# Kernel optimization log

Hardware: AMD Instinct MI355X
Metric: run time of the kernel (lower is better)

Reference implementation:

```python
import jax, jax.numpy as jnp
import numpy as np

N_NODES = 50000
N_EDGES_UND = 400000
N_GRAPHS = 128
LATENT = 64
OUT_DIM = 64
NODE_F = 64
EDGE_F = 32
MAX_LV = 3


def setup_inputs() -> dict:
    key = jax.random.key(0)
    ks = jax.random.split(key, 12)
    rng = np.random.default_rng(0)
    # Build consistent directed edge list: each undirected pair (u,v) yields
    # directed edges e (u->v) and e+E_und (v->u); rev maps each to its twin.
    u = rng.integers(0, N_NODES, size=N_EDGES_UND)
    v = rng.integers(0, N_NODES, size=N_EDGES_UND)
    src = jnp.asarray(np.concatenate([u, v]), dtype=jnp.int32)
    dst = jnp.asarray(np.concatenate([v, u]), dtype=jnp.int32)
    e = np.arange(N_EDGES_UND)
    rev = jnp.asarray(np.concatenate([e + N_EDGES_UND, e]), dtype=jnp.int32)
    graph_ids = jnp.sort(jax.random.randint(ks[0], (N_NODES,), 0, N_GRAPHS)).astype(jnp.int32)
    s = 0.05
    return {
        'node_feat': jax.random.normal(ks[1], (N_NODES, NODE_F), jnp.float32),
        'edge_feat': jax.random.normal(ks[2], (2 * N_EDGES_UND, EDGE_F), jnp.float32),
        'src': src, 'dst': dst, 'rev': rev,
        'graph_ids': graph_ids, 'n_graphs': N_GRAPHS,
        'Wn': jax.random.normal(ks[3], (NODE_F, LATENT), jnp.float32) * s,
        'bn': jnp.zeros((LATENT,), jnp.float32),
        'We': jax.random.normal(ks[4], (EDGE_F, LATENT), jnp.float32) * s,
        'be': jnp.zeros((LATENT,), jnp.float32),
        'Wc': jax.random.normal(ks[5], (LATENT, LATENT), jnp.float32) * s,
        'bc': jnp.zeros((LATENT,), jnp.float32),
        'Wo': jax.random.normal(ks[6], (LATENT, OUT_DIM), jnp.float32) * s,
        'bo': jnp.zeros((OUT_DIM,), jnp.float32),
    }


def reference(node_feat, edge_feat, src, dst, rev, graph_ids, n_graphs,
              Wn, bn, We, be, Wc, bc, Wo, bo):
    n_nodes = node_feat.shape[0]
    # w_n2l / w_e2l
    input_node_linear = node_feat @ Wn + bn                  # [N, D]
    input_edge_linear = edge_feat @ We + be                  # [E, D]
    # n2e spmm: each directed edge gathers its source node's row
    input_message = input_edge_linear + input_node_linear[src]  # [E, D]
    cur = jax.nn.relu(input_message)
    # loopy BP: e2e spmm = (sum of messages into src node) - reverse-edge message
    for _ in range(MAX_LV):
        node_agg = jax.ops.segment_sum(cur, dst, num_segments=n_nodes)  # [N, D]
        e2epool = node_agg[src] - cur[rev]                              # [E, D]
        cur = jax.nn.relu(e2epool @ Wc + bc + input_message)
    # e2n spmm: sum incoming edge messages per node
    e2npool = jax.ops.segment_sum(cur, dst, num_segments=n_nodes)       # [N, D]
    hidden_msg = jax.nn.relu(e2npool)
    reluact = jax.nn.relu(hidden_msg @ Wo + bo)                         # [N, out]
    # subg spmm: sum node outputs per graph
    y = jax.ops.segment_sum(reluact, graph_ids, num_segments=n_graphs)  # [G, out]
    return jax.nn.relu(y)
```

## Files before the change

### kernel.cpp

```cpp
#include <hip/hip_runtime.h>


#define NN 50000
#define NE 800000
#define NG 128
#define D 64
#define LDE 36
#define LDW 66
#define LDO 72

typedef unsigned short u16;
typedef unsigned int u32;
typedef __bf16 bf16x8 __attribute__((ext_vector_type(8)));
typedef float f32x4 __attribute__((ext_vector_type(4)));

__device__ __forceinline__ float b2f(u16 u){ u32 x=((u32)u)<<16; float f; __builtin_memcpy(&f,&x,4); return f; }
__device__ __forceinline__ u16 f2b(float f){ u32 x; __builtin_memcpy(&x,&f,4); x += 0x7fffu + ((x>>16)&1u); return (u16)(x>>16); }
__device__ __forceinline__ u32 pack2(float a, float b){ return (u32)f2b(a) | ((u32)f2b(b)<<16); }
__device__ __forceinline__ void unpack8(uint4 v, float* o){
  o[0]=b2f((u16)(v.x&0xffffu)); o[1]=b2f((u16)(v.x>>16));
  o[2]=b2f((u16)(v.y&0xffffu)); o[3]=b2f((u16)(v.y>>16));
  o[4]=b2f((u16)(v.z&0xffffu)); o[5]=b2f((u16)(v.z>>16));
  o[6]=b2f((u16)(v.w&0xffffu)); o[7]=b2f((u16)(v.w>>16));
}

__global__ __launch_bounds__(256) void k_prep(const float* __restrict__ Wc, const float* __restrict__ We,
                                              u16* __restrict__ wcB, u16* __restrict__ weB){
  int i = blockIdx.x*256 + threadIdx.x;
  if (i < 4096){
    int nt = i>>10, r = i&1023;
    int h = r>>9, r2 = r&511;
    int j = r2>>3, kk = r2&7;
    int row = nt*16 + (j&15);
    int k = h*32 + (j>>4)*8 + kk;
    wcB[i] = f2b(Wc[k*D + row]);
  }
  int t = i - 4096;
  if (t >= 0 && t < 2048){
    int nt = t>>9, r = t&511;
    int j = r>>3, kk = r&7;
    int row = nt*16 + (j&15);
    int k = (j>>4)*8 + kk;
    weB[t] = f2b(We[k*D + row]);
  }
}

template<int ZERO>
__global__ __launch_bounds__(256) void k_cvt(const float* __restrict__ srcv, u16* __restrict__ dstb,
                                             float* __restrict__ zbuf){
  size_t i = (size_t)(blockIdx.x*256 + threadIdx.x)*4;
  float4 v = *(const float4*)(srcv + i);
  *(uint2*)(dstb + i) = make_uint2(pack2(v.x,v.y), pack2(v.z,v.w));
  if (ZERO) *(float4*)(zbuf + i) = make_float4(0.f,0.f,0.f,0.f);
}

__global__ __launch_bounds__(256) void k_inl(const float* __restrict__ nf, const float* __restrict__ Wn,
                                             const float* __restrict__ bn, u16* __restrict__ inlb){
  __shared__ float w[D*D];
  for (int i=threadIdx.x;i<D*D;i+=256) w[i]=Wn[i];
  __syncthreads();
  const int d = threadIdx.x&63;
  const int n = blockIdx.x*4 + (threadIdx.x>>6);
  if (n>=NN) return;
  float v = bn[d];
  const float* row = nf + (size_t)n*D;
  #pragma unroll 8
  for (int k=0;k<D;k++) v += row[k]*w[k*D+d];
  inlb[(size_t)n*D+d] = f2b(v);
}

__global__ __launch_bounds__(256) void k_im(const float* __restrict__ ef, const u16* __restrict__ weB,
                                            const float* __restrict__ be, const u16* __restrict__ inlb,
                                            const int* __restrict__ src, const int* __restrict__ perm,
                                            u16* __restrict__ imP){
  __shared__ __align__(16) u16 efs[64*LDE];
  __shared__ float os[64*68];
  const int t = threadIdx.x;
  const int ebase = blockIdx.x*64;
  {
    int e=t>>2, k0=(t&3)*8;
    const float* p = ef + (size_t)(ebase+e)*32 + k0;
    float4 v0=*(const float4*)p, v1=*(const float4*)(p+4);
    uint4 pk = make_uint4(pack2(v0.x,v0.y),pack2(v0.z,v0.w),pack2(v1.x,v1.y),pack2(v1.z,v1.w));
    *(uint4*)&efs[e*LDE + k0] = pk;
  }
  {
    int w=t>>6, lane=t&63, q=lane>>4, mr=lane&15;
    int rowb=w*16;
    bf16x8 A = *(const bf16x8*)&efs[(rowb+mr)*LDE + q*8];
    #pragma unroll
    for (int nt=0;nt<4;nt++){
      bf16x8 B = *(const bf16x8*)(weB + nt*512 + lane*8);
      f32x4 acc = {0.f,0.f,0.f,0.f};
      acc = __builtin_amdgcn_mfma_f32_16x16x32_bf16(A,B,acc,0,0,0);
      #pragma unroll
      for (int r=0;r<4;r++) os[(rowb+q*4+r)*68 + nt*16+mr] = acc[r];
    }
  }
  {
    int e=t>>2, d0=(t&3)*16;
    const size_t eg = (size_t)(ebase+e);
    const int s = src[eg], ps = perm[eg];
    const u16* ip = inlb + (size_t)s*D + d0;
    uint4 iv0 = *(const uint4*)ip, iv1 = *(const uint4*)(ip+8);
    float il[16]; unpack8(iv0,il); unpack8(iv1,il+8);
    float x[16];
    #pragma unroll
    for (int j=0;j<16;j++) x[j] = os[e*68 + d0 + j] + be[d0+j] + il[j];
    uint4 p0 = make_uint4(pack2(x[0],x[1]),pack2(x[2],x[3]),pack2(x[4],x[5]),pack2(x[6],x[7]));
    uint4 p1 = make_uint4(pack2(x[8],x[9]),pack2(x[10],x[11]),pack2(x[12],x[13]),pack2(x[14],x[15]));
    u16* op = imP + (size_t)ps*D + d0;
    *(uint4*)op = p0; *(uint4*)(op+8) = p1;
  }
}

template<int MODE>
__global__ __launch_bounds__(256) void k_iter(const u16* __restrict__ imP, const u16* __restrict__ revIn,
      const u16* __restrict__ naWb, const u16* __restrict__ wcB, const float* __restrict__ bc,
      const int* __restrict__ srcP, const int* __restrict__ prevP, const int* __restrict__ nodeP,
      u16* __restrict__ revOut, float* __restrict__ naW_out){
  __shared__ __align__(16) u16 xs[64*LDW];
  __shared__ __align__(16) u16 os[64*LDO];
  __shared__ int nid[64];
  const int t = threadIdx.x;
  const int lane = t&63, w = t>>6;
  const size_t sbase = (size_t)blockIdx.x*64;
  if (lane < 16) nid[w*16 + lane] = nodeP[sbase + w*16 + lane];
  {
    const int e = t>>2, d0 = (t&3)*16;
    const size_t slot = sbase + e;
    const u16* ip = imP + slot*D + d0;
    uint4 r0 = *(const uint4*)ip, r1 = *(const uint4*)(ip+8);
    float x[16]; unpack8(r0,x); unpack8(r1,x+8);
    if (MODE == 1){
      const int sp = srcP[slot];
      const u16* cp = revIn + slot*D + d0;
      uint4 c0=*(const uint4*)cp, c1=*(const uint4*)(cp+8);
      const u16* np_ = naWb + (size_t)sp*D + d0;
      uint4 n0=*(const uint4*)np_, n1=*(const uint4*)(np_+8);
      float cv[16], nv[16];
      unpack8(c0,cv); unpack8(c1,cv+8);
      unpack8(n0,nv); unpack8(n1,nv+8);
      #pragma unroll
      for (int j=0;j<16;j++) x[j] += nv[j] - cv[j] + bc[d0+j];
    }
    #pragma unroll
    for (int j=0;j<16;j++) x[j] = x[j]>0.f ? x[j] : 0.f;
    uint4 p0 = make_uint4(pack2(x[0],x[1]),pack2(x[2],x[3]),pack2(x[4],x[5]),pack2(x[6],x[7]));
    uint4 p1 = make_uint4(pack2(x[8],x[9]),pack2(x[10],x[11]),pack2(x[12],x[13]),pack2(x[14],x[15]));
    u16* qd = &xs[e*LDW + d0];
    *(uint4*)qd = p0; *(uint4*)(qd+8) = p1;
  }
  {
    const int q = lane>>4, mr = lane&15;
    const int rowb = w*16;
    bf16x8 A0 = *(const bf16x8*)&xs[(rowb+mr)*LDW + q*8];
    bf16x8 A1 = *(const bf16x8*)&xs[(rowb+mr)*LDW + 32 + q*8];
    #pragma unroll
    for (int nt=0;nt<4;nt++){
      bf16x8 B0 = *(const bf16x8*)(wcB + nt*1024 + lane*8);
      bf16x8 B1 = *(const bf16x8*)(wcB + nt*1024 + 512 + lane*8);
      f32x4 acc = {0.f,0.f,0.f,0.f};
      acc = __builtin_amdgcn_mfma_f32_16x16x32_bf16(A0,B0,acc,0,0,0);
      acc = __builtin_amdgcn_mfma_f32_16x16x32_bf16(A1,B1,acc,0,0,0);
      #pragma unroll
      for (int r=0;r<4;r++) os[(rowb+q*4+r)*LDO + nt*16 + mr] = f2b(acc[r]);
    }
    const int lr = lane>>2, cc = lane&3;
    const int tgt = prevP[sbase + rowb + lr];
    u16* gp = revOut + (size_t)tgt*D + cc*16;
    *(uint4*)gp     = *(const uint4*)&os[(rowb+lr)*LDO + cc*16];
    *(uint4*)(gp+8) = *(const uint4*)&os[(rowb+lr)*LDO + cc*16 + 8];
    float acc = 0.f;
    int curn = nid[rowb];
    #pragma unroll 4
    for (int i=0;i<16;++i){
      int n = nid[rowb+i];
      if (n != curn){
        atomicAdd(&naW_out[(size_t)curn*D + lane], acc);
        curn = n; acc = 0.f;
      }
      acc += b2f(os[(rowb+i)*LDO + lane]);
    }
    atomicAdd(&naW_out[(size_t)curn*D + lane], acc);
  }
}

__global__ __launch_bounds__(256) void k_last(const u16* __restrict__ imP, const u16* __restrict__ revIn,
      const u16* __restrict__ naWb, const float* __restrict__ bc,
      const int* __restrict__ srcP, const int* __restrict__ nodeP,
      float* __restrict__ e2n){
  __shared__ __align__(16) u16 xs[64*LDW];
  __shared__ int nid[64];
  const int t = threadIdx.x;
  const int lane = t&63, w = t>>6;
  const size_t sbase = (size_t)blockIdx.x*64;
  if (lane < 16) nid[w*16+lane] = nodeP[sbase + w*16 + lane];
  {
    const int e = t>>2, d0 = (t&3)*16;
    const size_t slot = sbase + e;
    const u16* ip = imP + slot*D + d0;
    uint4 r0 = *(const uint4*)ip, r1 = *(const uint4*)(ip+8);
    float x[16]; unpack8(r0,x); unpack8(r1,x+8);
    const int sp = srcP[slot];
    const u16* cp = revIn + slot*D + d0;
    uint4 c0 = *(const uint4*)cp, c1 = *(const uint4*)(cp+8);
    const u16* np_ = naWb + (size_t)sp*D + d0;
    uint4 n0 = *(const uint4*)np_, n1 = *(const uint4*)(np_+8);
    float cv[16], nv[16];
    unpack8(c0,cv); unpack8(c1,cv+8);
    unpack8(n0,nv); unpack8(n1,nv+8);
    #pragma unroll
    for (int j=0;j<16;j++){ x[j] += nv[j] - cv[j] + bc[d0+j]; x[j] = x[j]>0.f ? x[j] : 0.f; }
    uint4 p0 = make_uint4(pack2(x[0],x[1]),pack2(x[2],x[3]),pack2(x[4],x[5]),pack2(x[6],x[7]));
    uint4 p1 = make_uint4(pack2(x[8],x[9]),pack2(x[10],x[11]),pack2(x[12],x[13]),pack2(x[14],x[15]));
    u16* qd = &xs[e*LDW + d0];
    *(uint4*)qd = p0; *(uint4*)(qd+8) = p1;
  }
  {
    float acc = 0.f;
    int curn = nid[w*16];
    #pragma unroll 4
    for (int i=0;i<16;++i){
      int n = nid[w*16+i];
      if (n != curn){
        atomicAdd(&e2n[(size_t)curn*D + lane], acc);
        curn = n; acc = 0.f;
      }
      acc += b2f(xs[(w*16+i)*LDW + lane]);
    }
    atomicAdd(&e2n[(size_t)curn*D + lane], acc);
  }
}

__global__ void k_hist(const int* __restrict__ dst, int* __restrict__ cnt){
  int e = blockIdx.x*256 + threadIdx.x;
  atomicAdd(&cnt[dst[e]], 1);
}
__global__ __launch_bounds__(1024) void k_scan1(const int* __restrict__ cnt, int* __restrict__ outv,
                                                int* __restrict__ bsums, int n){
  __shared__ int sh[1024];
  int i = blockIdx.x*1024 + threadIdx.x;
  int v = (i<n)? cnt[i] : 0;
  sh[threadIdx.x]=v;
  __syncthreads();
  for (int off=1; off<1024; off<<=1){
    int tv = (threadIdx.x>=(unsigned)off)? sh[threadIdx.x-off] : 0;
    __syncthreads();
    sh[threadIdx.x] += tv;
    __syncthreads();
  }
  if (i<n) outv[i] = sh[threadIdx.x] - v;
  if (threadIdx.x==1023) bsums[blockIdx.x] = sh[1023];
}
__global__ __launch_bounds__(1024) void k_scan3(int* __restrict__ off, int* __restrict__ cur,
                                                const int* __restrict__ bsums, int n){
  __shared__ int spref;
  if (threadIdx.x < 64){
    int v = ((int)threadIdx.x < (int)blockIdx.x) ? bsums[threadIdx.x] : 0;
    #pragma unroll
    for (int o=1;o<64;o<<=1) v += __shfl_xor(v, o, 64);
    if (threadIdx.x==0) spref = v;
  }
  __syncthreads();
  int i = blockIdx.x*1024 + threadIdx.x;
  if (i<n){ int v = off[i] + spref; off[i]=v; cur[i]=v; }
}
__global__ void k_fill(const int* __restrict__ dst, const int* __restrict__ src,
                       int* __restrict__ cur, int* __restrict__ perm,
                       int* __restrict__ srcP, int* __restrict__ nodeP){
  int e = blockIdx.x*256 + threadIdx.x;
  int d = dst[e];
  int pos = atomicAdd(&cur[d], 1);
  perm[e] = pos;
  srcP[pos] = src[e];
  nodeP[pos] = d;
}
__global__ void k_prev(const int* __restrict__ rev, const int* __restrict__ perm, int* __restrict__ prevP){
  int e = blockIdx.x*256 + threadIdx.x;
  prevP[perm[e]] = perm[rev[e]];
}

__global__ __launch_bounds__(256) void k_final(const float* __restrict__ e2n, const float* __restrict__ Wo,
                                               const float* __restrict__ bo, const int* __restrict__ gid,
                                               float* __restrict__ yacc){
  __shared__ float w[D*D];
  for (int i=threadIdx.x;i<D*D;i+=256) w[i]=Wo[i];
  __syncthreads();
  const int d = threadIdx.x&63, sub = threadIdx.x>>6;
  const int n0 = blockIdx.x*32 + sub*8;
  const float bod = bo[d];
  float acc=0.f; int curg=-1;
  for (int i=0;i<8;i++){
    int n=n0+i;
    if (n>=NN) break;
    int g = gid[n];
    if (g!=curg){ if (curg>=0) atomicAdd(&yacc[curg*D+d], acc); curg=g; acc=0.f; }
    float v=bod;
    const float* er = e2n + (size_t)n*D;
    #pragma unroll 8
    for (int k=0;k<D;k++){ float h=er[k]; h = h>0.f?h:0.f; v += h*w[k*D+d]; }
    acc += (v>0.f ? v : 0.f);
  }
  if (curg>=0) atomicAdd(&yacc[curg*D+d], acc);
}
__global__ void k_out(const float* __restrict__ yacc, float* __restrict__ outp){
  int i = blockIdx.x*256 + threadIdx.x;
  if (i<NG*D){ float v=yacc[i]; outp[i]= v>0.f?v:0.f; }
}

static constexpr size_t SZ_E   = (size_t)NE*D*2;
static constexpr size_t SZ_NF4 = (size_t)NN*D*4;
static constexpr size_t SZ_NB  = (size_t)NN*D*2;
static constexpr size_t OFF_IMP  = 0;
static constexpr size_t OFF_RVA  = SZ_E;
static constexpr size_t OFF_RVB  = 2*SZ_E;
static constexpr size_t OFF_CCUR = 3*SZ_E;
static constexpr size_t OFF_NA0  = OFF_CCUR + 200064;
static constexpr size_t OFF_NA1  = OFF_NA0 + SZ_NF4;
static constexpr size_t OFF_E2N  = OFF_NA1 + SZ_NF4;
static constexpr size_t OFF_YACC = OFF_E2N + SZ_NF4;
static constexpr size_t ZERO_SZ  = 200064 + 3*SZ_NF4 + (size_t)NG*D*4;
static constexpr size_t OFF_NAB  = OFF_YACC + (size_t)NG*D*4;
static constexpr size_t OFF_INL  = OFF_NAB + SZ_NB;
static constexpr size_t OFF_COFF = OFF_INL + SZ_NB;
static constexpr size_t OFF_PERM = OFF_COFF + 200064;
static constexpr size_t OFF_SRCP = OFF_PERM + (size_t)NE*4;
static constexpr size_t OFF_PRVP = OFF_SRCP + (size_t)NE*4;
static constexpr size_t OFF_NODP = OFF_PRVP + (size_t)NE*4;
static constexpr size_t OFF_BS   = OFF_NODP + (size_t)NE*4;
static constexpr size_t OFF_WCT  = OFF_BS + 256;
static constexpr size_t OFF_WET  = OFF_WCT + 8192;

extern "C" void kernel_launch(void* const* d_in, const int* in_sizes, int n_in,
                              void* d_out, int out_size, void* d_ws, size_t ws_size,
                              hipStream_t stream) {
  const float* node_feat = (const float*)d_in[0];
  const float* edge_feat = (const float*)d_in[1];
  const int*   src       = (const int*)d_in[2];
  const int*   dst       = (const int*)d_in[3];
  const int*   rev       = (const int*)d_in[4];
  const int*   gid       = (const int*)d_in[5];
  const float* Wn = (const float*)d_in[7];
  const float* bn = (const float*)d_in[8];
  const float* We = (const float*)d_in[9];
  const float* be = (const float*)d_in[10];
  const float* Wc = (const float*)d_in[11];
  const float* bc = (const float*)d_in[12];
  const float* Wo = (const float*)d_in[13];
  const float* bo = (const float*)d_in[14];

  char* ws = (char*)d_ws;
  u16*   imP     = (u16*)(ws + OFF_IMP);
  u16*   revA    = (u16*)(ws + OFF_RVA);
  u16*   revB    = (u16*)(ws + OFF_RVB);
  float* naW0    = (float*)(ws + OFF_NA0);
  float* naW1    = (float*)(ws + OFF_NA1);
  float* e2n     = (float*)(ws + OFF_E2N);
  float* yacc    = (float*)(ws + OFF_YACC);
  u16*   naWb    = (u16*)(ws + OFF_NAB);
  u16*   inlb    = (u16*)(ws + OFF_INL);
  int*   csr_off = (int*)(ws + OFF_COFF);
  int*   csr_cur = (int*)(ws + OFF_CCUR);
  int*   perm    = (int*)(ws + OFF_PERM);
  int*   srcP    = (int*)(ws + OFF_SRCP);
  int*   prevP   = (int*)(ws + OFF_PRVP);
  int*   nodeP   = (int*)(ws + OFF_NODP);
  int*   bsums   = (int*)(ws + OFF_BS);
  u16*   wcB     = (u16*)(ws + OFF_WCT);
  u16*   weB     = (u16*)(ws + OFF_WET);

  hipMemsetAsync(ws + OFF_CCUR, 0, ZERO_SZ, stream);

  k_hist <<<NE/256, 256, 0, stream>>>(dst, csr_cur);
  k_scan1<<<49, 1024, 0, stream>>>(csr_cur, csr_off, bsums, NN);
  k_scan3<<<49, 1024, 0, stream>>>(csr_off, csr_cur, bsums, NN);
  k_fill <<<NE/256, 256, 0, stream>>>(dst, src, csr_cur, perm, srcP, nodeP);
  k_prev <<<NE/256, 256, 0, stream>>>(rev, perm, prevP);

  k_prep<<<24, 256, 0, stream>>>(Wc, We, wcB, weB);
  k_inl <<<NN/4, 256, 0, stream>>>(node_feat, Wn, bn, inlb);
  k_im  <<<NE/64, 256, 0, stream>>>(edge_feat, weB, be, inlb, src, perm, imP);

  k_iter<0><<<NE/64, 256, 0, stream>>>(imP, revA, naWb, wcB, bc, srcP, prevP, nodeP, revA, naW0);
  k_cvt<0><<<3125, 256, 0, stream>>>(naW0, naWb, (float*)nullptr);
  k_iter<1><<<NE/64, 256, 0, stream>>>(imP, revA, naWb, wcB, bc, srcP, prevP, nodeP, revB, naW1);
  k_cvt<1><<<3125, 256, 0, stream>>>(naW1, naWb, naW0);
  k_iter<1><<<NE/64, 256, 0, stream>>>(imP, revB, naWb, wcB, bc, srcP, prevP, nodeP, revA, naW0);
  k_cvt<0><<<3125, 256, 0, stream>>>(naW0, naWb, (float*)nullptr);
  k_last<<<NE/64, 256, 0, stream>>>(imP, revA, naWb, bc, srcP, nodeP, e2n);

  k_final<<<(NN+31)/32, 256, 0, stream>>>(e2n, Wo, bo, gid, yacc);
  k_out<<<(NG*D)/256, 256, 0, stream>>>(yacc, (float*)d_out);
}
```

Baseline: 674.4 us.

## Replace atomic scatter aggregation with CSR pull-gather and pair-interleaved in-place edge updates

New measurement: 712.3 us. +5.6%, slower.

```diff
diff --git a/kernel.cpp b/kernel.cpp
--- a/kernel.cpp
+++ b/kernel.cpp
@@ -3,6 +3,7 @@
 
 #define NN 50000
 #define NE 800000
+#define NEU 400000
 #define NG 128
 #define D 64
 #define LDE 36
@@ -43,15 +44,6 @@
     int k = (j>>4)*8 + kk;
     weB[t] = f2b(We[k*D + row]);
   }
-}
-
-template<int ZERO>
-__global__ __launch_bounds__(256) void k_cvt(const float* __restrict__ srcv, u16* __restrict__ dstb,
-                                             float* __restrict__ zbuf){
-  size_t i = (size_t)(blockIdx.x*256 + threadIdx.x)*4;
-  float4 v = *(const float4*)(srcv + i);
-  *(uint2*)(dstb + i) = make_uint2(pack2(v.x,v.y), pack2(v.z,v.w));
-  if (ZERO) *(float4*)(zbuf + i) = make_float4(0.f,0.f,0.f,0.f);
 }
 
 __global__ __launch_bounds__(256) void k_inl(const float* __restrict__ nf, const float* __restrict__ Wn,
@@ -69,24 +61,24 @@
   inlb[(size_t)n*D+d] = f2b(v);
 }
 
-__global__ __launch_bounds__(256) void k_im(const float* __restrict__ ef, const u16* __restrict__ weB,
-                                            const float* __restrict__ be, const u16* __restrict__ inlb,
-                                            const int* __restrict__ src, const int* __restrict__ perm,
-                                            u16* __restrict__ imP){
+__global__ __launch_bounds__(256) void k_imf(const float* __restrict__ ef, const u16* __restrict__ weB,
+        const float* __restrict__ be, const u16* __restrict__ inlb, const int* __restrict__ src,
+        const u16* __restrict__ wcB, u16* __restrict__ imP, u16* __restrict__ yv){
   __shared__ __align__(16) u16 efs[64*LDE];
-  __shared__ float os[64*68];
+  __shared__ float osf[64*68];
+  __shared__ __align__(16) u16 xs[64*LDW];
+  __shared__ __align__(16) u16 osb[64*LDO];
   const int t = threadIdx.x;
+  const int lane = t&63, w = t>>6;
   const int ebase = blockIdx.x*64;
   {
     int e=t>>2, k0=(t&3)*8;
     const float* p = ef + (size_t)(ebase+e)*32 + k0;
     float4 v0=*(const float4*)p, v1=*(const float4*)(p+4);
-    uint4 pk = make_uint4(pack2(v0.x,v0.y),pack2(v0.z,v0.w),pack2(v1.x,v1.y),pack2(v1.z,v1.w));
-    *(uint4*)&efs[e*LDE + k0] = pk;
-  }
-  {
-    int w=t>>6, lane=t&63, q=lane>>4, mr=lane&15;
-    int rowb=w*16;
+    *(uint4*)&efs[e*LDE+k0] = make_uint4(pack2(v0.x,v0.y),pack2(v0.z,v0.w),pack2(v1.x,v1.y),pack2(v1.z,v1.w));
+  }
+  {
+    int q=lane>>4, mr=lane&15, rowb=w*16;
     bf16x8 A = *(const bf16x8*)&efs[(rowb+mr)*LDE + q*8];
     #pragma unroll
     for (int nt=0;nt<4;nt++){
@@ -94,61 +86,80 @@
       f32x4 acc = {0.f,0.f,0.f,0.f};
       acc = __builtin_amdgcn_mfma_f32_16x16x32_bf16(A,B,acc,0,0,0);
       #pragma unroll
-      for (int r=0;r<4;r++) os[(rowb+q*4+r)*68 + nt*16+mr] = acc[r];
+      for (int r=0;r<4;r++) osf[(rowb+q*4+r)*68 + nt*16+mr] = acc[r];
     }
   }
   {
     int e=t>>2, d0=(t&3)*16;
     const size_t eg = (size_t)(ebase+e);
-    const int s = src[eg], ps = perm[eg];
+    const int s = src[eg];
     const u16* ip = inlb + (size_t)s*D + d0;
     uint4 iv0 = *(const uint4*)ip, iv1 = *(const uint4*)(ip+8);
     float il[16]; unpack8(iv0,il); unpack8(iv1,il+8);
     float x[16];
     #pragma unroll
-    for (int j=0;j<16;j++) x[j] = os[e*68 + d0 + j] + be[d0+j] + il[j];
+    for (int j=0;j<16;j++) x[j] = osf[e*68 + d0 + j] + be[d0+j] + il[j];
     uint4 p0 = make_uint4(pack2(x[0],x[1]),pack2(x[2],x[3]),pack2(x[4],x[5]),pack2(x[6],x[7]));
     uint4 p1 = make_uint4(pack2(x[8],x[9]),pack2(x[10],x[11]),pack2(x[12],x[13]),pack2(x[14],x[15]));
-    u16* op = imP + (size_t)ps*D + d0;
+    u16* op = imP + eg*D + d0;
     *(uint4*)op = p0; *(uint4*)(op+8) = p1;
-  }
-}
-
-template<int MODE>
-__global__ __launch_bounds__(256) void k_iter(const u16* __restrict__ imP, const u16* __restrict__ revIn,
+    #pragma unroll
+    for (int j=0;j<16;j++) x[j] = x[j]>0.f ? x[j] : 0.f;
+    uint4 q0 = make_uint4(pack2(x[0],x[1]),pack2(x[2],x[3]),pack2(x[4],x[5]),pack2(x[6],x[7]));
+    uint4 q1 = make_uint4(pack2(x[8],x[9]),pack2(x[10],x[11]),pack2(x[12],x[13]),pack2(x[14],x[15]));
+    u16* qd = &xs[e*LDW + d0];
+    *(uint4*)qd = q0; *(uint4*)(qd+8) = q1;
+  }
+  {
+    const int q=lane>>4, mr=lane&15, rowb=w*16;
+    bf16x8 A0 = *(const bf16x8*)&xs[(rowb+mr)*LDW + q*8];
+    bf16x8 A1 = *(const bf16x8*)&xs[(rowb+mr)*LDW + 32 + q*8];
+    #pragma unroll
+    for (int nt=0;nt<4;nt++){
+      bf16x8 B0 = *(const bf16x8*)(wcB + nt*1024 + lane*8);
+      bf16x8 B1 = *(const bf16x8*)(wcB + nt*1024 + 512 + lane*8);
+      f32x4 acc = {0.f,0.f,0.f,0.f};
+      acc = __builtin_amdgcn_mfma_f32_16x16x32_bf16(A0,B0,acc,0,0,0);
+      acc = __builtin_amdgcn_mfma_f32_16x16x32_bf16(A1,B1,acc,0,0,0);
+      #pragma unroll
+      for (int r=0;r<4;r++) osb[(rowb+q*4+r)*LDO + nt*16 + mr] = f2b(acc[r]);
+    }
+    const int lr = lane>>2, cc = lane&3;
+    u16* gp = yv + (size_t)(ebase+rowb+lr)*D + cc*16;
+    *(uint4*)gp     = *(const uint4*)&osb[(rowb+lr)*LDO + cc*16];
+    *(uint4*)(gp+8) = *(const uint4*)&osb[(rowb+lr)*LDO + cc*16 + 8];
+  }
+}
+
+__global__ __launch_bounds__(256) void k_iter_pi(const u16* __restrict__ imP, u16* __restrict__ yv,
       const u16* __restrict__ naWb, const u16* __restrict__ wcB, const float* __restrict__ bc,
-      const int* __restrict__ srcP, const int* __restrict__ prevP, const int* __restrict__ nodeP,
-      u16* __restrict__ revOut, float* __restrict__ naW_out){
+      const int* __restrict__ src){
   __shared__ __align__(16) u16 xs[64*LDW];
   __shared__ __align__(16) u16 os[64*LDO];
-  __shared__ int nid[64];
   const int t = threadIdx.x;
   const int lane = t&63, w = t>>6;
-  const size_t sbase = (size_t)blockIdx.x*64;
-  if (lane < 16) nid[w*16 + lane] = nodeP[sbase + w*16 + lane];
-  {
-    const int e = t>>2, d0 = (t&3)*16;
-    const size_t slot = sbase + e;
-    const u16* ip = imP + slot*D + d0;
-    uint4 r0 = *(const uint4*)ip, r1 = *(const uint4*)(ip+8);
-    float x[16]; unpack8(r0,x); unpack8(r1,x+8);
-    if (MODE == 1){
-      const int sp = srcP[slot];
-      const u16* cp = revIn + slot*D + d0;
-      uint4 c0=*(const uint4*)cp, c1=*(const uint4*)(cp+8);
-      const u16* np_ = naWb + (size_t)sp*D + d0;
-      uint4 n0=*(const uint4*)np_, n1=*(const uint4*)(np_+8);
-      float cv[16], nv[16];
-      unpack8(c0,cv); unpack8(c1,cv+8);
-      unpack8(n0,nv); unpack8(n1,nv+8);
-      #pragma unroll
-      for (int j=0;j<16;j++) x[j] += nv[j] - cv[j] + bc[d0+j];
-    }
-    #pragma unroll
-    for (int j=0;j<16;j++) x[j] = x[j]>0.f ? x[j] : 0.f;
+  const int pbase = blockIdx.x*32 + w*8;
+  {
+    const int rr = lane>>2, d0 = (lane&3)*16;
+    const int pr = pbase + (rr&7);
+    const int e   = (rr<8)? pr : NEU+pr;
+    const int etw = (rr<8)? NEU+pr : pr;
+    const int sp = src[e];
+    const u16* ip = imP + (size_t)e*D + d0;
+    uint4 r0=*(const uint4*)ip, r1=*(const uint4*)(ip+8);
+    const u16* cp = yv + (size_t)etw*D + d0;
+    uint4 c0=*(const uint4*)cp, c1=*(const uint4*)(cp+8);
+    const u16* np_ = naWb + (size_t)sp*D + d0;
+    uint4 n0=*(const uint4*)np_, n1=*(const uint4*)(np_+8);
+    float x[16], cv[16], nv[16];
+    unpack8(r0,x); unpack8(r1,x+8);
+    unpack8(c0,cv); unpack8(c1,cv+8);
+    unpack8(n0,nv); unpack8(n1,nv+8);
+    #pragma unroll
+    for (int j=0;j<16;j++){ x[j] += nv[j] - cv[j] + bc[d0+j]; x[j] = x[j]>0.f ? x[j] : 0.f; }
     uint4 p0 = make_uint4(pack2(x[0],x[1]),pack2(x[2],x[3]),pack2(x[4],x[5]),pack2(x[6],x[7]));
     uint4 p1 = make_uint4(pack2(x[8],x[9]),pack2(x[10],x[11]),pack2(x[12],x[13]),pack2(x[14],x[15]));
-    u16* qd = &xs[e*LDW + d0];
+    u16* qd = &xs[(w*16+rr)*LDW + d0];
     *(uint4*)qd = p0; *(uint4*)(qd+8) = p1;
   }
   {
@@ -167,70 +178,70 @@
       for (int r=0;r<4;r++) os[(rowb+q*4+r)*LDO + nt*16 + mr] = f2b(acc[r]);
     }
     const int lr = lane>>2, cc = lane&3;
-    const int tgt = prevP[sbase + rowb + lr];
-    u16* gp = revOut + (size_t)tgt*D + cc*16;
+    const int pr2 = pbase + (lr&7);
+    const int e2 = (lr<8)? pr2 : NEU+pr2;
+    u16* gp = yv + (size_t)e2*D + cc*16;
     *(uint4*)gp     = *(const uint4*)&os[(rowb+lr)*LDO + cc*16];
     *(uint4*)(gp+8) = *(const uint4*)&os[(rowb+lr)*LDO + cc*16 + 8];
-    float acc = 0.f;
-    int curn = nid[rowb];
-    #pragma unroll 4
-    for (int i=0;i<16;++i){
-      int n = nid[rowb+i];
-      if (n != curn){
-        atomicAdd(&naW_out[(size_t)curn*D + lane], acc);
-        curn = n; acc = 0.f;
-      }
-      acc += b2f(os[(rowb+i)*LDO + lane]);
-    }
-    atomicAdd(&naW_out[(size_t)curn*D + lane], acc);
-  }
-}
-
-__global__ __launch_bounds__(256) void k_last(const u16* __restrict__ imP, const u16* __restrict__ revIn,
-      const u16* __restrict__ naWb, const float* __restrict__ bc,
-      const int* __restrict__ srcP, const int* __restrict__ nodeP,
-      float* __restrict__ e2n){
-  __shared__ __align__(16) u16 xs[64*LDW];
-  __shared__ int nid[64];
+  }
+}
+
+__global__ __launch_bounds__(256) void k_last_pi(const u16* __restrict__ imP, u16* __restrict__ yv,
+      const u16* __restrict__ naWb, const float* __restrict__ bc, const int* __restrict__ src){
   const int t = threadIdx.x;
   const int lane = t&63, w = t>>6;
-  const size_t sbase = (size_t)blockIdx.x*64;
-  if (lane < 16) nid[w*16+lane] = nodeP[sbase + w*16 + lane];
-  {
-    const int e = t>>2, d0 = (t&3)*16;
-    const size_t slot = sbase + e;
-    const u16* ip = imP + slot*D + d0;
-    uint4 r0 = *(const uint4*)ip, r1 = *(const uint4*)(ip+8);
-    float x[16]; unpack8(r0,x); unpack8(r1,x+8);
-    const int sp = srcP[slot];
-    const u16* cp = revIn + slot*D + d0;
-    uint4 c0 = *(const uint4*)cp, c1 = *(const uint4*)(cp+8);
-    const u16* np_ = naWb + (size_t)sp*D + d0;
-    uint4 n0 = *(const uint4*)np_, n1 = *(const uint4*)(np_+8);
-    float cv[16], nv[16];
-    unpack8(c0,cv); unpack8(c1,cv+8);
-    unpack8(n0,nv); unpack8(n1,nv+8);
-    #pragma unroll
-    for (int j=0;j<16;j++){ x[j] += nv[j] - cv[j] + bc[d0+j]; x[j] = x[j]>0.f ? x[j] : 0.f; }
-    uint4 p0 = make_uint4(pack2(x[0],x[1]),pack2(x[2],x[3]),pack2(x[4],x[5]),pack2(x[6],x[7]));
-    uint4 p1 = make_uint4(pack2(x[8],x[9]),pack2(x[10],x[11]),pack2(x[12],x[13]),pack2(x[14],x[15]));
-    u16* qd = &xs[e*LDW + d0];
-    *(uint4*)qd = p0; *(uint4*)(qd+8) = p1;
-  }
-  {
-    float acc = 0.f;
-    int curn = nid[w*16];
-    #pragma unroll 4
-    for (int i=0;i<16;++i){
-      int n = nid[w*16+i];
-      if (n != curn){
-        atomicAdd(&e2n[(size_t)curn*D + lane], acc);
-        curn = n; acc = 0.f;
+  const int pbase = blockIdx.x*32 + w*8;
+  const int rr = lane>>2, d0 = (lane&3)*16;
+  const int pr = pbase + (rr&7);
+  const int e   = (rr<8)? pr : NEU+pr;
+  const int etw = (rr<8)? NEU+pr : pr;
+  const int sp = src[e];
+  const u16* ip = imP + (size_t)e*D + d0;
+  uint4 r0=*(const uint4*)ip, r1=*(const uint4*)(ip+8);
+  const u16* cp = yv + (size_t)etw*D + d0;
+  uint4 c0=*(const uint4*)cp, c1=*(const uint4*)(cp+8);
+  const u16* np_ = naWb + (size_t)sp*D + d0;
+  uint4 n0=*(const uint4*)np_, n1=*(const uint4*)(np_+8);
+  float x[16], cv[16], nv[16];
+  unpack8(r0,x); unpack8(r1,x+8);
+  unpack8(c0,cv); unpack8(c1,cv+8);
+  unpack8(n0,nv); unpack8(n1,nv+8);
+  #pragma unroll
+  for (int j=0;j<16;j++){ x[j] += nv[j] - cv[j] + bc[d0+j]; x[j] = x[j]>0.f ? x[j] : 0.f; }
+  uint4 p0 = make_uint4(pack2(x[0],x[1]),pack2(x[2],x[3]),pack2(x[4],x[5]),pack2(x[6],x[7]));
+  uint4 p1 = make_uint4(pack2(x[8],x[9]),pack2(x[10],x[11]),pack2(x[12],x[13]),pack2(x[14],x[15]));
+  u16* gp = yv + (size_t)e*D + d0;
+  *(uint4*)gp = p0; *(uint4*)(gp+8) = p1;
+}
+
+template<int F32OUT>
+__global__ __launch_bounds__(256) void k_agg(const u16* __restrict__ yv, const int* __restrict__ offs,
+        const int* __restrict__ ends, const int* __restrict__ csrE,
+        u16* __restrict__ outb, float* __restrict__ outf){
+  const int lane = threadIdx.x&63, w = threadIdx.x>>6;
+  const int n = blockIdx.x*4 + w;
+  if (n >= NN) return;
+  int t0 = offs[n]; const int e_ = ends[n];
+  float acc = 0.f;
+  while (t0 < e_){
+    int chunk = e_ - t0; if (chunk > 64) chunk = 64;
+    int myidx = csrE[t0 + ((lane < chunk) ? lane : 0)];
+    int j = 0;
+    for (; j+8 <= chunk; j += 8){
+      #pragma unroll
+      for (int u=0;u<8;u++){
+        int e = __shfl(myidx, j+u, 64);
+        acc += b2f(yv[(size_t)e*D + lane]);
       }
-      acc += b2f(xs[(w*16+i)*LDW + lane]);
-    }
-    atomicAdd(&e2n[(size_t)curn*D + lane], acc);
-  }
+    }
+    for (; j < chunk; ++j){
+      int e = __shfl(myidx, j, 64);
+      acc += b2f(yv[(size_t)e*D + lane]);
+    }
+    t0 += chunk;
+  }
+  if (F32OUT) outf[(size_t)n*D + lane] = acc;
+  else        outb[(size_t)n*D + lane] = f2b(acc);
 }
 
 __global__ void k_hist(const int* __restrict__ dst, int* __restrict__ cnt){
@@ -266,19 +277,10 @@
   int i = blockIdx.x*1024 + threadIdx.x;
   if (i<n){ int v = off[i] + spref; off[i]=v; cur[i]=v; }
 }
-__global__ void k_fill(const int* __restrict__ dst, const int* __restrict__ src,
-                       int* __restrict__ cur, int* __restrict__ perm,
-                       int* __restrict__ srcP, int* __restrict__ nodeP){
+__global__ void k_fill(const int* __restrict__ dst, int* __restrict__ cur, int* __restrict__ csrE){
   int e = blockIdx.x*256 + threadIdx.x;
-  int d = dst[e];
-  int pos = atomicAdd(&cur[d], 1);
-  perm[e] = pos;
-  srcP[pos] = src[e];
-  nodeP[pos] = d;
-}
-__global__ void k_prev(const int* __restrict__ rev, const int* __restrict__ perm, int* __restrict__ prevP){
-  int e = blockIdx.x*256 + threadIdx.x;
-  prevP[perm[e]] = perm[rev[e]];
+  int pos = atomicAdd(&cur[dst[e]], 1);
+  csrE[pos] = e;
 }
 
 __global__ __launch_bounds__(256) void k_final(const float* __restrict__ e2n, const float* __restrict__ Wo,
@@ -313,22 +315,16 @@
 static constexpr size_t SZ_NF4 = (size_t)NN*D*4;
 static constexpr size_t SZ_NB  = (size_t)NN*D*2;
 static constexpr size_t OFF_IMP  = 0;
-static constexpr size_t OFF_RVA  = SZ_E;
-static constexpr size_t OFF_RVB  = 2*SZ_E;
-static constexpr size_t OFF_CCUR = 3*SZ_E;
-static constexpr size_t OFF_NA0  = OFF_CCUR + 200064;
-static constexpr size_t OFF_NA1  = OFF_NA0 + SZ_NF4;
-static constexpr size_t OFF_E2N  = OFF_NA1 + SZ_NF4;
-static constexpr size_t OFF_YACC = OFF_E2N + SZ_NF4;
-static constexpr size_t ZERO_SZ  = 200064 + 3*SZ_NF4 + (size_t)NG*D*4;
-static constexpr size_t OFF_NAB  = OFF_YACC + (size_t)NG*D*4;
+static constexpr size_t OFF_YV   = SZ_E;
+static constexpr size_t OFF_CCUR = 2*SZ_E;
+static constexpr size_t OFF_YACC = OFF_CCUR + 200064;
+static constexpr size_t ZERO_SZ  = 200064 + (size_t)NG*D*4;
+static constexpr size_t OFF_E2N  = OFF_YACC + (size_t)NG*D*4;
+static constexpr size_t OFF_NAB  = OFF_E2N + SZ_NF4;
 static constexpr size_t OFF_INL  = OFF_NAB + SZ_NB;
 static constexpr size_t OFF_COFF = OFF_INL + SZ_NB;
-static constexpr size_t OFF_PERM = OFF_COFF + 200064;
-static constexpr size_t OFF_SRCP = OFF_PERM + (size_t)NE*4;
-static constexpr size_t OFF_PRVP = OFF_SRCP + (size_t)NE*4;
-static constexpr size_t OFF_NODP = OFF_PRVP + (size_t)NE*4;
-static constexpr size_t OFF_BS   = OFF_NODP + (size_t)NE*4;
+static constexpr size_t OFF_CSRE = OFF_COFF + 200064;
+static constexpr size_t OFF_BS   = OFF_CSRE + (size_t)NE*4;
 static constexpr size_t OFF_WCT  = OFF_BS + 256;
 static constexpr size_t OFF_WET  = OFF_WCT + 8192;
 
@@ -339,7 +335,6 @@
   const float* edge_feat = (const float*)d_in[1];
   const int*   src       = (const int*)d_in[2];
   const int*   dst       = (const int*)d_in[3];
-  const int*   rev       = (const int*)d_in[4];
   const int*   gid       = (const int*)d_in[5];
   const float* Wn = (const float*)d_in[7];
   const float* bn = (const float*)d_in[8];
@@ -352,20 +347,14 @@
 
   char* ws = (char*)d_ws;
   u16*   imP     = (u16*)(ws + OFF_IMP);
-  u16*   revA    = (u16*)(ws + OFF_RVA);
-  u16*   revB    = (u16*)(ws + OFF_RVB);
-  float* naW0    = (float*)(ws + OFF_NA0);
-  float* naW1    = (float*)(ws + OFF_NA1);
+  u16*   yv      = (u16*)(ws + OFF_YV);
   float* e2n     = (float*)(ws + OFF_E2N);
   float* yacc    = (float*)(ws + OFF_YACC);
   u16*   naWb    = (u16*)(ws + OFF_NAB);
   u16*   inlb    = (u16*)(ws + OFF_INL);
   int*   csr_off = (int*)(ws + OFF_COFF);
   int*   csr_cur = (int*)(ws + OFF_CCUR);
-  int*   perm    = (int*)(ws + OFF_PERM);
-  int*   srcP    = (int*)(ws + OFF_SRCP);
-  int*   prevP   = (int*)(ws + OFF_PRVP);
-  int*   nodeP   = (int*)(ws + OFF_NODP);
+  int*   csrE    = (int*)(ws + OFF_CSRE);
   int*   bsums   = (int*)(ws + OFF_BS);
   u16*   wcB     = (u16*)(ws + OFF_WCT);
   u16*   weB     = (u16*)(ws + OFF_WET);
@@ -375,20 +364,19 @@
   k_hist <<<NE/256, 256, 0, stream>>>(dst, csr_cur);
   k_scan1<<<49, 1024, 0, stream>>>(csr_cur, csr_off, bsums, NN);
   k_scan3<<<49, 1024, 0, stream>>>(csr_off, csr_cur, bsums, NN);
-  k_fill <<<NE/256, 256, 0, stream>>>(dst, src, csr_cur, perm, srcP, nodeP);
-  k_prev <<<NE/256, 256, 0, stream>>>(rev, perm, prevP);
+  k_fill <<<NE/256, 256, 0, stream>>>(dst, csr_cur, csrE);
 
   k_prep<<<24, 256, 0, stream>>>(Wc, We, wcB, weB);
   k_inl <<<NN/4, 256, 0, stream>>>(node_feat, Wn, bn, inlb);
-  k_im  <<<NE/64, 256, 0, stream>>>(edge_feat, weB, be, inlb, src, perm, imP);
-
-  k_iter<0><<<NE/64, 256, 0, stream>>>(imP, revA, naWb, wcB, bc, srcP, prevP, nodeP, revA, naW0);
-  k_cvt<0><<<3125, 256, 0, stream>>>(naW0, naWb, (float*)nullptr);
-  k_iter<1><<<NE/64, 256, 0, stream>>>(imP, revA, naWb, wcB, bc, srcP, prevP, nodeP, revB, naW1);
-  k_cvt<1><<<3125, 256, 0, stream>>>(naW1, naWb, naW0);
-  k_iter<1><<<NE/64, 256, 0, stream>>>(imP, revB, naWb, wcB, bc, srcP, prevP, nodeP, revA, naW0);
-  k_cvt<0><<<3125, 256, 0, stream>>>(naW0, naWb, (float*)nullptr);
-  k_last<<<NE/64, 256, 0, stream>>>(imP, revA, naWb, bc, srcP, nodeP, e2n);
+  k_imf <<<NE/64, 256, 0, stream>>>(edge_feat, weB, be, inlb, src, wcB, imP, yv);
+
+  k_agg<0><<<NN/4, 256, 0, stream>>>(yv, csr_off, csr_cur, csrE, naWb, (float*)nullptr);
+  k_iter_pi<<<NE/64, 256, 0, stream>>>(imP, yv, naWb, wcB, bc, src);
+  k_agg<0><<<NN/4, 256, 0, stream>>>(yv, csr_off, csr_cur, csrE, naWb, (float*)nullptr);
+  k_iter_pi<<<NE/64, 256, 0, stream>>>(imP, yv, naWb, wcB, bc, src);
+  k_agg<0><<<NN/4, 256, 0, stream>>>(yv, csr_off, csr_cur, csrE, naWb, (float*)nullptr);
+  k_last_pi<<<NE/64, 256, 0, stream>>>(imP, yv, naWb, bc, src);
+  k_agg<1><<<NN/4, 256, 0, stream>>>(yv, csr_off, csr_cur, csrE, (u16*)nullptr, e2n);
 
   k_final<<<(NN+31)/32, 256, 0, stream>>>(e2n, Wo, bo, gid, yacc);
   k_out<<<(NG*D)/256, 256, 0, stream>>>(yacc, (float*)d_out);
```

## Fuse input-message kernel with first iteration and switch reverse writes to gathered reads

Applied to the files above, without the earlier changes.

Result: slower. 697.3 us (+3.4%).

```diff
diff --git a/kernel.cpp b/kernel.cpp
--- a/kernel.cpp
+++ b/kernel.cpp
@@ -69,24 +69,28 @@
   inlb[(size_t)n*D+d] = f2b(v);
 }
 
-__global__ __launch_bounds__(256) void k_im(const float* __restrict__ ef, const u16* __restrict__ weB,
-                                            const float* __restrict__ be, const u16* __restrict__ inlb,
-                                            const int* __restrict__ src, const int* __restrict__ perm,
-                                            u16* __restrict__ imP){
+__global__ __launch_bounds__(256) void k_imf2(const float* __restrict__ ef, const u16* __restrict__ weB,
+        const float* __restrict__ be, const u16* __restrict__ inlb, const int* __restrict__ srcP,
+        const int* __restrict__ eP, const int* __restrict__ nodeP, const u16* __restrict__ wcB,
+        u16* __restrict__ imP, u16* __restrict__ revOut, float* __restrict__ naW_out){
   __shared__ __align__(16) u16 efs[64*LDE];
-  __shared__ float os[64*68];
+  __shared__ float osf[64*68];
+  __shared__ __align__(16) u16 xs[64*LDW];
+  __shared__ __align__(16) u16 osb[64*LDO];
+  __shared__ int nid[64];
   const int t = threadIdx.x;
-  const int ebase = blockIdx.x*64;
-  {
-    int e=t>>2, k0=(t&3)*8;
-    const float* p = ef + (size_t)(ebase+e)*32 + k0;
+  const int lane = t&63, w = t>>6;
+  const size_t sbase = (size_t)blockIdx.x*64;
+  if (lane < 16) nid[w*16 + lane] = nodeP[sbase + w*16 + lane];
+  {
+    int r=t>>2, k0=(t&3)*8;
+    const int e = eP[sbase + r];
+    const float* p = ef + (size_t)e*32 + k0;
     float4 v0=*(const float4*)p, v1=*(const float4*)(p+4);
-    uint4 pk = make_uint4(pack2(v0.x,v0.y),pack2(v0.z,v0.w),pack2(v1.x,v1.y),pack2(v1.z,v1.w));
-    *(uint4*)&efs[e*LDE + k0] = pk;
-  }
-  {
-    int w=t>>6, lane=t&63, q=lane>>4, mr=lane&15;
-    int rowb=w*16;
+    *(uint4*)&efs[r*LDE+k0] = make_uint4(pack2(v0.x,v0.y),pack2(v0.z,v0.w),pack2(v1.x,v1.y),pack2(v1.z,v1.w));
+  }
+  {
+    int q=lane>>4, mr=lane&15, rowb=w*16;
     bf16x8 A = *(const bf16x8*)&efs[(rowb+mr)*LDE + q*8];
     #pragma unroll
     for (int nt=0;nt<4;nt++){
@@ -94,28 +98,65 @@
       f32x4 acc = {0.f,0.f,0.f,0.f};
       acc = __builtin_amdgcn_mfma_f32_16x16x32_bf16(A,B,acc,0,0,0);
       #pragma unroll
-      for (int r=0;r<4;r++) os[(rowb+q*4+r)*68 + nt*16+mr] = acc[r];
-    }
-  }
-  {
-    int e=t>>2, d0=(t&3)*16;
-    const size_t eg = (size_t)(ebase+e);
-    const int s = src[eg], ps = perm[eg];
+      for (int r=0;r<4;r++) osf[(rowb+q*4+r)*68 + nt*16+mr] = acc[r];
+    }
+  }
+  {
+    int r=t>>2, d0=(t&3)*16;
+    const size_t slot = sbase + r;
+    const int s = srcP[slot];
     const u16* ip = inlb + (size_t)s*D + d0;
     uint4 iv0 = *(const uint4*)ip, iv1 = *(const uint4*)(ip+8);
     float il[16]; unpack8(iv0,il); unpack8(iv1,il+8);
     float x[16];
     #pragma unroll
-    for (int j=0;j<16;j++) x[j] = os[e*68 + d0 + j] + be[d0+j] + il[j];
+    for (int j=0;j<16;j++) x[j] = osf[r*68 + d0 + j] + be[d0+j] + il[j];
     uint4 p0 = make_uint4(pack2(x[0],x[1]),pack2(x[2],x[3]),pack2(x[4],x[5]),pack2(x[6],x[7]));
     uint4 p1 = make_uint4(pack2(x[8],x[9]),pack2(x[10],x[11]),pack2(x[12],x[13]),pack2(x[14],x[15]));
-    u16* op = imP + (size_t)ps*D + d0;
+    u16* op = imP + slot*D + d0;
     *(uint4*)op = p0; *(uint4*)(op+8) = p1;
-  }
-}
-
-template<int MODE>
-__global__ __launch_bounds__(256) void k_iter(const u16* __restrict__ imP, const u16* __restrict__ revIn,
+    #pragma unroll
+    for (int j=0;j<16;j++) x[j] = x[j]>0.f ? x[j] : 0.f;
+    uint4 q0 = make_uint4(pack2(x[0],x[1]),pack2(x[2],x[3]),pack2(x[4],x[5]),pack2(x[6],x[7]));
+    uint4 q1 = make_uint4(pack2(x[8],x[9]),pack2(x[10],x[11]),pack2(x[12],x[13]),pack2(x[14],x[15]));
+    u16* qd = &xs[r*LDW + d0];
+    *(uint4*)qd = q0; *(uint4*)(qd+8) = q1;
+  }
+  {
+    const int q = lane>>4, mr = lane&15;
+    const int rowb = w*16;
+    bf16x8 A0 = *(const bf16x8*)&xs[(rowb+mr)*LDW + q*8];
+    bf16x8 A1 = *(const bf16x8*)&xs[(rowb+mr)*LDW + 32 + q*8];
+    #pragma unroll
+    for (int nt=0;nt<4;nt++){
+      bf16x8 B0 = *(const bf16x8*)(wcB + nt*1024 + lane*8);
+      bf16x8 B1 = *(const bf16x8*)(wcB + nt*1024 + 512 + lane*8);
+      f32x4 acc = {0.f,0.f,0.f,0.f};
+      acc = __builtin_amdgcn_mfma_f32_16x16x32_bf16(A0,B0,acc,0,0,0);
+      acc = __builtin_amdgcn_mfma_f32_16x16x32_bf16(A1,B1,acc,0,0,0);
+      #pragma unroll
+      for (int r=0;r<4;r++) osb[(rowb+q*4+r)*LDO + nt*16 + mr] = f2b(acc[r]);
+    }
+    const int lr = lane>>2, cc = lane&3;
+    u16* gp = revOut + (sbase + rowb + lr)*D + cc*16;
+    *(uint4*)gp     = *(const uint4*)&osb[(rowb+lr)*LDO + cc*16];
+    *(uint4*)(gp+8) = *(const uint4*)&osb[(rowb+lr)*LDO + cc*16 + 8];
+    float acc = 0.f;
+    int curn = nid[rowb];
+    #pragma unroll 4
+    for (int i=0;i<16;++i){
+      int n = nid[rowb+i];
+      if (n != curn){
+        atomicAdd(&naW_out[(size_t)curn*D + lane], acc);
+        curn = n; acc = 0.f;
+      }
+      acc += b2f(osb[(rowb+i)*LDO + lane]);
+    }
+    atomicAdd(&naW_out[(size_t)curn*D + lane], acc);
+  }
+}
+
+__global__ __launch_bounds__(256) void k_iter1(const u16* __restrict__ imP, const u16* __restrict__ revIn,
       const u16* __restrict__ naWb, const u16* __restrict__ wcB, const float* __restrict__ bc,
       const int* __restrict__ srcP, const int* __restrict__ prevP, const int* __restrict__ nodeP,
       u16* __restrict__ revOut, float* __restrict__ naW_out){
@@ -132,20 +173,17 @@
     const u16* ip = imP + slot*D + d0;
     uint4 r0 = *(const uint4*)ip, r1 = *(const uint4*)(ip+8);
     float x[16]; unpack8(r0,x); unpack8(r1,x+8);
-    if (MODE == 1){
-      const int sp = srcP[slot];
-      const u16* cp = revIn + slot*D + d0;
-      uint4 c0=*(const uint4*)cp, c1=*(const uint4*)(cp+8);
-      const u16* np_ = naWb + (size_t)sp*D + d0;
-      uint4 n0=*(const uint4*)np_, n1=*(const uint4*)(np_+8);
-      float cv[16], nv[16];
-      unpack8(c0,cv); unpack8(c1,cv+8);
-      unpack8(n0,nv); unpack8(n1,nv+8);
-      #pragma unroll
-      for (int j=0;j<16;j++) x[j] += nv[j] - cv[j] + bc[d0+j];
-    }
-    #pragma unroll
-    for (int j=0;j<16;j++) x[j] = x[j]>0.f ? x[j] : 0.f;
+    const int sp = srcP[slot];
+    const int tw = prevP[slot];
+    const u16* cp = revIn + (size_t)tw*D + d0;
+    uint4 c0=*(const uint4*)cp, c1=*(const uint4*)(cp+8);
+    const u16* np_ = naWb + (size_t)sp*D + d0;
+    uint4 n0=*(const uint4*)np_, n1=*(const uint4*)(np_+8);
+    float cv[16], nv[16];
+    unpack8(c0,cv); unpack8(c1,cv+8);
+    unpack8(n0,nv); unpack8(n1,nv+8);
+    #pragma unroll
+    for (int j=0;j<16;j++){ x[j] += nv[j] - cv[j] + bc[d0+j]; x[j] = x[j]>0.f ? x[j] : 0.f; }
     uint4 p0 = make_uint4(pack2(x[0],x[1]),pack2(x[2],x[3]),pack2(x[4],x[5]),pack2(x[6],x[7]));
     uint4 p1 = make_uint4(pack2(x[8],x[9]),pack2(x[10],x[11]),pack2(x[12],x[13]),pack2(x[14],x[15]));
     u16* qd = &xs[e*LDW + d0];
@@ -167,8 +205,7 @@
       for (int r=0;r<4;r++) os[(rowb+q*4+r)*LDO + nt*16 + mr] = f2b(acc[r]);
     }
     const int lr = lane>>2, cc = lane&3;
-    const int tgt = prevP[sbase + rowb + lr];
-    u16* gp = revOut + (size_t)tgt*D + cc*16;
+    u16* gp = revOut + (sbase + rowb + lr)*D + cc*16;
     *(uint4*)gp     = *(const uint4*)&os[(rowb+lr)*LDO + cc*16];
     *(uint4*)(gp+8) = *(const uint4*)&os[(rowb+lr)*LDO + cc*16 + 8];
     float acc = 0.f;
@@ -188,7 +225,7 @@
 
 __global__ __launch_bounds__(256) void k_last(const u16* __restrict__ imP, const u16* __restrict__ revIn,
       const u16* __restrict__ naWb, const float* __restrict__ bc,
-      const int* __restrict__ srcP, const int* __restrict__ nodeP,
+      const int* __restrict__ srcP, const int* __restrict__ prevP, const int* __restrict__ nodeP,
       float* __restrict__ e2n){
   __shared__ __align__(16) u16 xs[64*LDW];
   __shared__ int nid[64];
@@ -203,7 +240,8 @@
     uint4 r0 = *(const uint4*)ip, r1 = *(const uint4*)(ip+8);
     float x[16]; unpack8(r0,x); unpack8(r1,x+8);
     const int sp = srcP[slot];
-    const u16* cp = revIn + slot*D + d0;
+    const int tw = prevP[slot];
+    const u16* cp = revIn + (size_t)tw*D + d0;
     uint4 c0 = *(const uint4*)cp, c1 = *(const uint4*)(cp+8);
     const u16* np_ = naWb + (size_t)sp*D + d0;
     uint4 n0 = *(const uint4*)np_, n1 = *(const uint4*)(np_+8);
@@ -268,13 +306,14 @@
 }
 __global__ void k_fill(const int* __restrict__ dst, const int* __restrict__ src,
                        int* __restrict__ cur, int* __restrict__ perm,
-                       int* __restrict__ srcP, int* __restrict__ nodeP){
+                       int* __restrict__ srcP, int* __restrict__ nodeP, int* __restrict__ eP){
   int e = blockIdx.x*256 + threadIdx.x;
   int d = dst[e];
   int pos = atomicAdd(&cur[d], 1);
   perm[e] = pos;
   srcP[pos] = src[e];
   nodeP[pos] = d;
+  eP[pos] = e;
 }
 __global__ void k_prev(const int* __restrict__ rev, const int* __restrict__ perm, int* __restrict__ prevP){
   int e = blockIdx.x*256 + threadIdx.x;
@@ -328,7 +367,8 @@
 static constexpr size_t OFF_SRCP = OFF_PERM + (size_t)NE*4;
 static constexpr size_t OFF_PRVP = OFF_SRCP + (size_t)NE*4;
 static constexpr size_t OFF_NODP = OFF_PRVP + (size_t)NE*4;
-static constexpr size_t OFF_BS   = OFF_NODP + (size_t)NE*4;
+static constexpr size_t OFF_EP   = OFF_NODP + (size_t)NE*4;
+static constexpr size_t OFF_BS   = OFF_EP + (size_t)NE*4;
 static constexpr size_t OFF_WCT  = OFF_BS + 256;
 static constexpr size_t OFF_WET  = OFF_WCT + 8192;
 
@@ -366,6 +406,7 @@
   int*   srcP    = (int*)(ws + OFF_SRCP);
   int*   prevP   = (int*)(ws + OFF_PRVP);
   int*   nodeP   = (int*)(ws + OFF_NODP);
+  int*   eP      = (int*)(ws + OFF_EP);
   int*   bsums   = (int*)(ws + OFF_BS);
   u16*   wcB     = (u16*)(ws + OFF_WCT);
   u16*   weB     = (u16*)(ws + OFF_WET);
@@ -375,20 +416,20 @@
   k_hist <<<NE/256, 256, 0, stream>>>(dst, csr_cur);
   k_scan1<<<49, 1024, 0, stream>>>(csr_cur, csr_off, bsums, NN);
   k_scan3<<<49, 1024, 0, stream>>>(csr_off, csr_cur, bsums, NN);
-  k_fill <<<NE/256, 256, 0, stream>>>(dst, src, csr_cur, perm, srcP, nodeP);
+  k_fill <<<NE/256, 256, 0, stream>>>(dst, src, csr_cur, perm, srcP, nodeP, eP);
   k_prev <<<NE/256, 256, 0, stream>>>(rev, perm, prevP);
 
   k_prep<<<24, 256, 0, stream>>>(Wc, We, wcB, weB);
   k_inl <<<NN/4, 256, 0, stream>>>(node_feat, Wn, bn, inlb);
-  k_im  <<<NE/64, 256, 0, stream>>>(edge_feat, weB, be, inlb, src, perm, imP);
-
-  k_iter<0><<<NE/64, 256, 0, stream>>>(imP, revA, naWb, wcB, bc, srcP, prevP, nodeP, revA, naW0);
+
+  k_imf2<<<NE/64, 256, 0, stream>>>(edge_feat, weB, be, inlb, srcP, eP, nodeP, wcB, imP, revA, naW0);
+
   k_cvt<0><<<3125, 256, 0, stream>>>(naW0, naWb, (float*)nullptr);
-  k_iter<1><<<NE/64, 256, 0, stream>>>(imP, revA, naWb, wcB, bc, srcP, prevP, nodeP, revB, naW1);
+  k_iter1<<<NE/64, 256, 0, stream>>>(imP, revA, naWb, wcB, bc, srcP, prevP, nodeP, revB, naW1);
   k_cvt<1><<<3125, 256, 0, stream>>>(naW1, naWb, naW0);
-  k_iter<1><<<NE/64, 256, 0, stream>>>(imP, revB, naWb, wcB, bc, srcP, prevP, nodeP, revA, naW0);
+  k_iter1<<<NE/64, 256, 0, stream>>>(imP, revB, naWb, wcB, bc, srcP, prevP, nodeP, revA, naW0);
   k_cvt<0><<<3125, 256, 0, stream>>>(naW0, naWb, (float*)nullptr);
-  k_last<<<NE/64, 256, 0, stream>>>(imP, revA, naWb, bc, srcP, nodeP, e2n);
+  k_last<<<NE/64, 256, 0, stream>>>(imP, revA, naWb, bc, srcP, prevP, nodeP, e2n);
 
   k_final<<<(NN+31)/32, 256, 0, stream>>>(e2n, Wo, bo, gid, yacc);
   k_out<<<(NG*D)/256, 256, 0, stream>>>(yacc, (float*)d_out);
```
